# Optimization experiments

Hardware: AMD Instinct MI355X
Metric: run time of the kernel (lower is better)

## Reference

```python
import jax, jax.numpy as jnp
import numpy as np

PAD = 4  # init_kwargs pad


def setup_inputs() -> dict:
    key = jax.random.key(0)
    k1, k2 = jax.random.split(key)
    x = jax.random.normal(k1, (1024, 4, 84, 84), dtype=jnp.float32)
    shift = jax.random.randint(k2, (1024, 1, 1, 2), 0, 2 * PAD + 1, dtype=jnp.int32)
    return {"x": x, "shift": shift}


def _random_shift_aug(x, shift, pad):
    n, c, h, w = x.shape
    # replicate pad on H and W (matches F.pad(..., 'replicate'))
    xp = jnp.pad(x, ((0, 0), (0, 0), (pad, pad), (pad, pad)), mode='edge')
    Hp, Wp = h + 2 * pad, w + 2 * pad

    # base grid: normalized centers of the first w/h pixels of the padded image
    eps_x = 1.0 / Wp
    ax = jnp.linspace(-1.0 + eps_x, 1.0 - eps_x, Wp, dtype=x.dtype)[:w]  # (w,)
    eps_y = 1.0 / (h + 2 * 4)  # NOTE: original code hardcodes 4 here, not pad
    ay = jnp.linspace(-1.0 + eps_y, 1.0 - eps_y, h + 2 * 4, dtype=x.dtype)[:h]  # (h,)

    scale = jnp.asarray(2.0 / (h + 2 * pad), dtype=x.dtype)
    sx = shift[..., 0].astype(x.dtype) * scale  # (n,1,1)
    sy = shift[..., 1].astype(x.dtype) * scale  # (n,1,1)

    gx = ax[None, None, :] + sx  # (n,1,w) normalized x coords
    gy = ay[None, :, None] + sy  # (n,h,1) normalized y coords

    # grid_sample unnormalization, align_corners=False
    ix = ((gx + 1.0) * Wp - 1.0) * 0.5  # (n,1,w)
    iy = ((gy + 1.0) * Hp - 1.0) * 0.5  # (n,h,1)

    ix0f = jnp.floor(ix)
    iy0f = jnp.floor(iy)
    wx = (ix - ix0f)[..., None]  # (n,1,w,1)
    wy = (iy - iy0f)[..., None]  # (n,h,1,1)
    ix0 = ix0f.astype(jnp.int32)
    iy0 = iy0f.astype(jnp.int32)

    b = jnp.arange(n, dtype=jnp.int32)[:, None, None]  # (n,1,1)

    def corner(iyi, ixi):
        # zeros padding_mode: mask out-of-bounds taps
        valid = ((ixi >= 0) & (ixi < Wp) & (iyi >= 0) & (iyi < Hp)).astype(x.dtype)
        v = xp[b, :, jnp.clip(iyi, 0, Hp - 1), jnp.clip(ixi, 0, Wp - 1)]  # (n,h,w,c)
        return v * valid[..., None]

    v00 = corner(iy0, ix0)
    v01 = corner(iy0, ix0 + 1)
    v10 = corner(iy0 + 1, ix0)
    v11 = corner(iy0 + 1, ix0 + 1)

    out = (v00 * (1 - wy) * (1 - wx) + v01 * (1 - wy) * wx
           + v10 * wy * (1 - wx) + v11 * wy * wx)  # (n,h,w,c)
    return jnp.transpose(out, (0, 3, 1, 2))  # (n,c,h,w)


def reference(x, shift):
    return _random_shift_aug(x, shift, PAD)
```

## Files before the change

### kernel.cpp

```cpp
#include <hip/hip_runtime.h>


#define HW 84
#define WQ 21
#define RPB 12
#define PADV 4
#define PLANE (HW * HW)
#define IMG_ELEMS (4 * PLANE)

__global__ __launch_bounds__(WQ * RPB)
void shift_aug_kernel(const float* __restrict__ x,
                      const int* __restrict__ shift,
                      float* __restrict__ out) {
    __shared__ float lds[RPB][HW];

    const int tx = threadIdx.x;
    const int ty = threadIdx.y;
    const int bx = blockIdx.x;
    const int n  = blockIdx.y;

    const int c    = bx / 7;
    const int band = (bx - c * 7) * RPB;

    const int sx = shift[2 * n]     - PADV;
    const int sy = shift[2 * n + 1] - PADV;

    const int h  = band + ty;
    const int sh = min(max(h + sy, 0), HW - 1);

    const float* __restrict__ plane = x + (size_t)n * IMG_ELEMS + (size_t)c * PLANE;

    float4 L = ((const float4*)(plane + sh * HW))[tx];
    ((float4*)&lds[ty][0])[tx] = L;
    __syncthreads();

    const int wb = 4 * tx + sx;
    float4 v;
    v.x = lds[ty][min(max(wb + 0, 0), HW - 1)];
    v.y = lds[ty][min(max(wb + 1, 0), HW - 1)];
    v.z = lds[ty][min(max(wb + 2, 0), HW - 1)];
    v.w = lds[ty][min(max(wb + 3, 0), HW - 1)];

    float* __restrict__ oplane = out + (size_t)n * IMG_ELEMS + (size_t)c * PLANE;
    ((float4*)(oplane + h * HW))[tx] = v;
}

extern "C" void kernel_launch(void* const* d_in, const int* in_sizes, int n_in,
                              void* d_out, int out_size, void* d_ws, size_t ws_size,
                              hipStream_t stream) {
    const float* x     = (const float*)d_in[0];
    const int*   shift = (const int*)d_in[1];
    float*       out   = (float*)d_out;

    dim3 block(WQ, RPB, 1);
    dim3 grid(28, 1024, 1);
    shift_aug_kernel<<<grid, block, 0, stream>>>(x, shift, out);
}
```

Baseline: 196.8 us.

## Process whole plane per block with wave-local LDS rows and prefetched loads

Each block now handles a full 84x84 plane (one block per image-channel) with four 64-lane waves, each wave owning three rows per band, looping over seven bands. The next band's row is prefetched into registers while the current one is written to a padded, double-buffered LDS row. Edge replication is baked into LDS pad slots so the shifted read becomes two float4 LDS loads plus a lane-select, and block-wide syncs are replaced by wave barriers. This cuts block count and per-block launch overhead, but leaves one lane idle per wave (63 of 64 active) and adds register pressure from the unrolled loop.

New measurement: 208.1 us. +5.8%, slower.

```diff
diff --git a/kernel.cpp b/kernel.cpp
--- a/kernel.cpp
+++ b/kernel.cpp
@@ -2,47 +2,75 @@
 
 
 #define HW 84
-#define WQ 21
-#define RPB 12
 #define PADV 4
 #define PLANE (HW * HW)
-#define IMG_ELEMS (4 * PLANE)
+#define LROW 92
+#define BANDS 7
 
-__global__ __launch_bounds__(WQ * RPB)
+__global__ __launch_bounds__(256)
 void shift_aug_kernel(const float* __restrict__ x,
                       const int* __restrict__ shift,
                       float* __restrict__ out) {
-    __shared__ float lds[RPB][HW];
+    __shared__ float lds[4][2][3][LROW];
 
-    const int tx = threadIdx.x;
-    const int ty = threadIdx.y;
-    const int bx = blockIdx.x;
-    const int n  = blockIdx.y;
+    const int lane = threadIdx.x;
+    const int w    = threadIdx.y;
+    const int b    = blockIdx.x;
 
-    const int c    = bx / 7;
-    const int band = (bx - c * 7) * RPB;
-
+    const int n  = b >> 2;
     const int sx = shift[2 * n]     - PADV;
     const int sy = shift[2 * n + 1] - PADV;
+    const int s4 = sx + PADV;
+    const int q  = s4 >> 2;
+    const int r  = s4 & 3;
 
-    const int h  = band + ty;
-    const int sh = min(max(h + sy, 0), HW - 1);
+    const int j  = lane / 21;
+    const int tx = lane - j * 21;
+    const bool active = (lane < 63);
 
-    const float* __restrict__ plane = x + (size_t)n * IMG_ELEMS + (size_t)c * PLANE;
+    const float* __restrict__ plane  = x   + (size_t)b * PLANE;
+    float*       __restrict__ oplane = out + (size_t)b * PLANE;
 
-    float4 L = ((const float4*)(plane + sh * HW))[tx];
-    ((float4*)&lds[ty][0])[tx] = L;
-    __syncthreads();
+    const int rbase = w * 3 + j;
 
-    const int wb = 4 * tx + sx;
-    float4 v;
-    v.x = lds[ty][min(max(wb + 0, 0), HW - 1)];
-    v.y = lds[ty][min(max(wb + 1, 0), HW - 1)];
-    v.z = lds[ty][min(max(wb + 2, 0), HW - 1)];
-    v.w = lds[ty][min(max(wb + 3, 0), HW - 1)];
+    float4 L = make_float4(0.f, 0.f, 0.f, 0.f);
+    {
+        const int sh = min(max(rbase + sy, 0), HW - 1);
+        if (active) L = ((const float4*)(plane + sh * HW))[tx];
+    }
 
-    float* __restrict__ oplane = out + (size_t)n * IMG_ELEMS + (size_t)c * PLANE;
-    ((float4*)(oplane + h * HW))[tx] = v;
+    #pragma unroll
+    for (int t = 0; t < BANDS; ++t) {
+        float4 Ln = L;
+        if (t + 1 < BANDS) {
+            const int sh1 = min(max((t + 1) * 12 + rbase + sy, 0), HW - 1);
+            if (active) Ln = ((const float4*)(plane + sh1 * HW))[tx];
+        }
+
+        float* row = &lds[w][t & 1][j][0];
+        if (active) {
+            ((float4*)row)[1 + tx] = L;
+            if (tx == 0)  ((float4*)row)[0]  = make_float4(L.x, L.x, L.x, L.x);
+            if (tx == 20) ((float4*)row)[22] = make_float4(L.w, L.w, L.w, L.w);
+        }
+        __builtin_amdgcn_wave_barrier();
+
+        if (active) {
+            const float4* row4 = (const float4*)row;
+            const float4 a = row4[tx + q];
+            float4 o;
+            if (r == 0) {
+                o = a;
+            } else {
+                const float4 bb = row4[tx + q + 1];
+                if (r == 1)      o = make_float4(a.y, a.z, a.w, bb.x);
+                else if (r == 2) o = make_float4(a.z, a.w, bb.x, bb.y);
+                else             o = make_float4(a.w, bb.x, bb.y, bb.z);
+            }
+            ((float4*)(oplane + (t * 12 + rbase) * HW))[tx] = o;
+        }
+        L = Ln;
+    }
 }
 
 extern "C" void kernel_launch(void* const* d_in, const int* in_sizes, int n_in,
@@ -52,7 +80,7 @@
     const int*   shift = (const int*)d_in[1];
     float*       out   = (float*)d_out;
 
-    dim3 block(WQ, RPB, 1);
-    dim3 grid(28, 1024, 1);
+    dim3 block(64, 4, 1);
+    dim3 grid(4096, 1, 1);
     shift_aug_kernel<<<grid, block, 0, stream>>>(x, shift, out);
 }
```

## Process whole plane per block with unaligned register loads, drop LDS

Applied to the files above, without the earlier changes.

Each block now handles one full 84x84 plane with 256 threads, each doing 7 float4 outputs. The kernel no longer stages a row in LDS and synchronizes. It loads an unaligned 4-float window directly from global memory at the clamped shifted position and selects lanes in registers for replicate padding. This removes the LDS round trip, the barrier and the small 252-thread blocks, and gives more loads in flight per thread. In exchange the global loads are misaligned (4-byte aligned) and the last iteration wastes some lanes.

New measurement: 200.7 us. About the same (+2.0%).

```diff
diff --git a/kernel.cpp b/kernel.cpp
--- a/kernel.cpp
+++ b/kernel.cpp
@@ -2,47 +2,68 @@
 
 
 #define HW 84
-#define WQ 21
-#define RPB 12
 #define PADV 4
 #define PLANE (HW * HW)
-#define IMG_ELEMS (4 * PLANE)
+#define PF4   (PLANE / 4)
+#define NTHR  256
+#define K     7
 
-__global__ __launch_bounds__(WQ * RPB)
+struct __attribute__((aligned(4))) f4u { float x, y, z, w; };
+
+__device__ __forceinline__ float pick(const f4u& v, int idx) {
+    return (idx < 1) ? v.x : (idx < 2) ? v.y : (idx < 3) ? v.z : v.w;
+}
+
+__global__ __launch_bounds__(NTHR)
 void shift_aug_kernel(const float* __restrict__ x,
                       const int* __restrict__ shift,
                       float* __restrict__ out) {
-    __shared__ float lds[RPB][HW];
-
-    const int tx = threadIdx.x;
-    const int ty = threadIdx.y;
-    const int bx = blockIdx.x;
-    const int n  = blockIdx.y;
-
-    const int c    = bx / 7;
-    const int band = (bx - c * 7) * RPB;
+    const int tid = threadIdx.x;
+    const int b   = blockIdx.x;
+    const int n   = b >> 2;
 
     const int sx = shift[2 * n]     - PADV;
     const int sy = shift[2 * n + 1] - PADV;
 
-    const int h  = band + ty;
-    const int sh = min(max(h + sy, 0), HW - 1);
+    const float* __restrict__ plane  = x   + (size_t)b * PLANE;
+    float*       __restrict__ oplane = out + (size_t)b * PLANE;
 
-    const float* __restrict__ plane = x + (size_t)n * IMG_ELEMS + (size_t)c * PLANE;
+    int src[K];
+    int dsel[K];
 
-    float4 L = ((const float4*)(plane + sh * HW))[tx];
-    ((float4*)&lds[ty][0])[tx] = L;
-    __syncthreads();
+    #pragma unroll
+    for (int i = 0; i < K; ++i) {
+        const int g   = tid + NTHR * i;
+        const int gi  = (g < PF4) ? g : (PF4 - 1);
+        const int row = gi / 21;
+        const int tx  = gi - row * 21;
+        const int srow = min(max(row + sy, 0), HW - 1);
+        const int cb   = 4 * tx + sx;
+        const int B    = min(max(cb, 0), HW - 4);
+        src[i]  = srow * HW + B;
+        dsel[i] = cb - B;
+    }
 
-    const int wb = 4 * tx + sx;
-    float4 v;
-    v.x = lds[ty][min(max(wb + 0, 0), HW - 1)];
-    v.y = lds[ty][min(max(wb + 1, 0), HW - 1)];
-    v.z = lds[ty][min(max(wb + 2, 0), HW - 1)];
-    v.w = lds[ty][min(max(wb + 3, 0), HW - 1)];
+    f4u L[K];
+    #pragma unroll
+    for (int i = 0; i < K; ++i)
+        L[i] = *(const f4u*)(plane + src[i]);
 
-    float* __restrict__ oplane = out + (size_t)n * IMG_ELEMS + (size_t)c * PLANE;
-    ((float4*)(oplane + h * HW))[tx] = v;
+    #pragma unroll
+    for (int i = 0; i < K; ++i) {
+        const int d = dsel[i];
+        float4 o;
+        o.x = pick(L[i], min(max(d,     0), 3));
+        o.y = pick(L[i], min(max(d + 1, 0), 3));
+        o.z = pick(L[i], min(max(d + 2, 0), 3));
+        o.w = pick(L[i], min(max(d + 3, 0), 3));
+        const int g = tid + NTHR * i;
+        if (i < K - 1) {
+            ((float4*)oplane)[g] = o;
+        } else if (g < PF4) {
+            ((float4*)oplane)[g] = o;
+        }
+    }
 }
 
 extern "C" void kernel_launch(void* const* d_in, const int* in_sizes, int n_in,
@@ -52,7 +73,7 @@
     const int*   shift = (const int*)d_in[1];
     float*       out   = (float*)d_out;
 
-    dim3 block(WQ, RPB, 1);
-    dim3 grid(28, 1024, 1);
+    dim3 block(NTHR, 1, 1);
+    dim3 grid(4096, 1, 1);
     shift_aug_kernel<<<grid, block, 0, stream>>>(x, shift, out);
 }
```
